# Performance work log

Measured on AMD Instinct MI355X. Metric: run time of the kernel, lower is better.

The kernel has to match this reference:

```python
import jax, jax.numpy as jnp
import numpy as np

N, C, H, W = 8, 192, 64, 64
CQK = 24  # C // ratio with ratio=8


def setup_inputs() -> dict:
    key = jax.random.key(0)
    k1, k2, k3, k4 = jax.random.split(key, 4)
    x = jax.random.normal(k1, (N, C, H, W), dtype=jnp.float32)
    Wq = jax.random.normal(k2, (CQK, C), dtype=jnp.float32) * (1.0 / np.sqrt(C))
    Wk = jax.random.normal(k3, (CQK, C), dtype=jnp.float32) * (1.0 / np.sqrt(C))
    Wv = jax.random.normal(k4, (C, C), dtype=jnp.float32) * (1.0 / np.sqrt(C))
    return {"x": x, "Wq": Wq, "Wk": Wk, "Wv": Wv}


def reference(x, Wq, Wk, Wv):
    n, c, h, w = x.shape
    xf = x.reshape(n, c, h * w)                       # [n, C, L]
    q = jnp.einsum('oc,ncl->nol', Wq, xf)             # [n, CQK, L] (1x1 conv)
    k = jnp.einsum('oc,ncl->nol', Wk, xf)             # [n, CQK, L]
    v = jnp.einsum('oc,ncl->nol', Wv, xf)             # [n, C, L]
    # mask[n, l, m] = softmax_m( q[:, :, l] . k[:, :, m] )  -- no scaling in original
    scores = jnp.einsum('nol,nom->nlm', q, k)         # [n, L, L]
    mask = jax.nn.softmax(scores, axis=-1)
    # feat = v @ mask^T : feat[n, c, l] = sum_m v[n, c, m] * mask[n, l, m]
    feat = jnp.einsum('ncm,nlm->ncl', v, mask)
    return feat.reshape(n, c, h, w)
```

## Files before the change

### kernel.cpp

```cpp
#include <hip/hip_runtime.h>
#include <hip/hip_bf16.h>

#define L 4096
#define NB 8
#define C 192
#define CQK 24
#define DP 32
#define QBLK 64
#define KBLK 64
#define NT (L / KBLK)
#define BN 64
#define XS_W 200
#define LOG2E 1.4426950408889634f

typedef _Float16 half_t;
typedef __fp16 fp16x2 __attribute__((ext_vector_type(2)));
typedef __fp16 fp16x4 __attribute__((ext_vector_type(4)));
typedef _Float16 half8 __attribute__((ext_vector_type(8)));
typedef float f32x4 __attribute__((ext_vector_type(4)));


__global__ __launch_bounds__(256, 2) void proj_mfma(const float* __restrict__ x,
                                                    const float* __restrict__ Wq,
                                                    const float* __restrict__ Wk,
                                                    const float* __restrict__ Wv,
                                                    half_t* __restrict__ Qh,
                                                    half_t* __restrict__ Kh,
                                                    half_t* __restrict__ Vh) {
  __shared__ half_t Xs[BN][XS_W];
  __shared__ half_t Qt[BN][DP];
  __shared__ half_t Kt[BN][DP];

  int tid = threadIdx.x;
  int lane = tid & 63;
  int wave = tid >> 6;
  int li = lane & 15;
  int g = lane >> 4;

  int blk = blockIdx.x;
  int n = blk >> 6;
  int l0 = (blk & 63) * BN;

  const float* xbase = x + (size_t)n * C * L + l0;
#pragma unroll
  for (int it = 0; it < 12; ++it) {
    int fid = it * 256 + tid;
    int l4 = fid & 15;
    int c = fid >> 4;
    f32x4 v = *reinterpret_cast<const f32x4*>(xbase + (size_t)c * L + l4 * 4);
#pragma unroll
    for (int j = 0; j < 4; ++j) Xs[l4 * 4 + j][c] = (half_t)v[j];
  }
  __syncthreads();

  const float* rowp[4];
  bool rvalid[4];
#pragma unroll
  for (int mt = 0; mt < 4; ++mt) {
    int row = wave * 64 + mt * 16 + li;
    const float* p;
    bool v = true;
    if (row < 32) {
      v = row < CQK;
      p = Wq + (size_t)(v ? row : 0) * C;
    } else if (row < 64) {
      v = (row - 32) < CQK;
      p = Wk + (size_t)(v ? row - 32 : 0) * C;
    } else {
      p = Wv + (size_t)(row - 64) * C;
    }
    rowp[mt] = p;
    rvalid[mt] = v;
  }

  f32x4 acc[4][4];
#pragma unroll
  for (int mt = 0; mt < 4; ++mt)
#pragma unroll
    for (int nt = 0; nt < 4; ++nt) acc[mt][nt] = {0.f, 0.f, 0.f, 0.f};

  half8 az;
#pragma unroll
  for (int j = 0; j < 8; ++j) az[j] = (half_t)0.f;

#pragma unroll
  for (int kk = 0; kk < 6; ++kk) {
    half8 af[4];
#pragma unroll
    for (int mt = 0; mt < 4; ++mt) {
      const float* p = rowp[mt] + kk * 32 + g * 8;
      f32x4 w0 = *reinterpret_cast<const f32x4*>(p);
      f32x4 w1 = *reinterpret_cast<const f32x4*>(p + 4);
      half8 a;
#pragma unroll
      for (int j = 0; j < 4; ++j) {
        a[j] = (half_t)w0[j];
        a[4 + j] = (half_t)w1[j];
      }
      af[mt] = rvalid[mt] ? a : az;
    }
#pragma unroll
    for (int nt = 0; nt < 4; ++nt) {
      half8 b = *reinterpret_cast<const half8*>(&Xs[nt * 16 + li][kk * 32 + g * 8]);
#pragma unroll
      for (int mt = 0; mt < 4; ++mt)
        acc[mt][nt] = __builtin_amdgcn_mfma_f32_16x16x32_f16(af[mt], b, acc[mt][nt], 0, 0, 0);
    }
  }

  if (wave >= 1) {
#pragma unroll
    for (int mt = 0; mt < 4; ++mt)
#pragma unroll
      for (int nt = 0; nt < 4; ++nt)
#pragma unroll
        for (int r = 0; r < 4; ++r) {
          int c = (wave - 1) * 64 + mt * 16 + 4 * g + r;
          int l = nt * 16 + li;
          Vh[((size_t)n * C + c) * L + l0 + l] = (half_t)acc[mt][nt][r];
        }
  } else {
#pragma unroll
    for (int mt = 0; mt < 4; ++mt)
#pragma unroll
      for (int nt = 0; nt < 4; ++nt)
#pragma unroll
        for (int r = 0; r < 4; ++r) {
          int o = (mt & 1) * 16 + 4 * g + r;
          int l = nt * 16 + li;
          if (mt < 2) Qt[l][o] = (half_t)(acc[mt][nt][r] * LOG2E);
          else        Kt[l][o] = (half_t)acc[mt][nt][r];
        }
  }
  __syncthreads();

  if (tid < 128) {
    int which = tid >> 6;
    int l = tid & 63;
    const half8* src = reinterpret_cast<const half8*>(which ? &Kt[l][0] : &Qt[l][0]);
    half_t* dstp = (which ? Kh : Qh) + ((size_t)n * L + l0 + l) * DP;
    half8* dst = reinterpret_cast<half8*>(dstp);
#pragma unroll
    for (int i = 0; i < 4; ++i) dst[i] = src[i];
  }
}


struct SMemA {
  half_t P[2][QBLK][KBLK];
  float rs[2][QBLK];
  float Ls[QBLK];
};

__global__ __launch_bounds__(256, 2) void attn(const half_t* __restrict__ Qh,
                                               const half_t* __restrict__ Kh,
                                               const half_t* __restrict__ Vh,
                                               float* __restrict__ out) {
  __shared__ SMemA sm;

  const int tid = threadIdx.x;
  const int wave = tid >> 6;
  const int lane = tid & 63;
  const int li = lane & 15;
  const int g = lane >> 4;
  const int n = blockIdx.x;
  const int q0 = blockIdx.y * QBLK;
  const int c0 = wave * 48;
  const int swz = (li & 7) << 4;

  const half8 qfrag = *reinterpret_cast<const half8*>(
      Qh + ((size_t)(n * L + q0 + wave * 16 + li)) * DP + g * 8);

  const char* kptr = (const char*)(Kh + (size_t)n * L * DP) +
                     ((size_t)li * DP + g * 8) * 2;
  const char* vb[3];
  vb[0] = (const char*)(Vh + (size_t)n * C * L) +
          ((size_t)(c0 + li) * L + g * 8) * 2;
  vb[1] = vb[0] + (size_t)16 * L * 2;
  vb[2] = vb[0] + (size_t)32 * L * 2;

  f32x4 acc[3][4];
#pragma unroll
  for (int ct = 0; ct < 3; ++ct)
#pragma unroll
    for (int qt = 0; qt < 4; ++qt) acc[ct][qt] = {0.f, 0.f, 0.f, 0.f};

  float Lrow = 0.f;
  float coff = -28.f;

  half8 kA[4], vA[6], kB[4], vB[6];

  auto sm_write = [&](const f32x4(&s)[4], int par) {
    float p[4][4];
    float mx = -1.0e30f;
#pragma unroll
    for (int b = 0; b < 4; ++b) {
      mx = fmaxf(mx, fmaxf(fmaxf(s[b][0], s[b][1]), fmaxf(s[b][2], s[b][3])));
#pragma unroll
      for (int r = 0; r < 4; ++r) p[b][r] = __builtin_amdgcn_exp2f(s[b][r]);
    }
    float sc = 1.0f;
    if (__any((int)(mx > 15.f))) {
      float m2 = fmaxf(mx, __shfl_xor(mx, 16));
      m2 = fmaxf(m2, __shfl_xor(m2, 32));
      if (m2 > 15.f) {
        sc = __builtin_amdgcn_exp2f(-m2);
        Lrow *= sc;
        coff -= m2;
#pragma unroll
        for (int b = 0; b < 4; ++b)
#pragma unroll
          for (int r = 0; r < 4; ++r)
            p[b][r] = __builtin_amdgcn_exp2f(s[b][r] - m2);
      }
    }
#pragma unroll
    for (int b = 0; b < 4; ++b)
#pragma unroll
      for (int r = 0; r < 4; ++r) Lrow += p[b][r];

    char* prow = (char*)&sm.P[par][wave * 16 + li][0];
#pragma unroll
    for (int b = 0; b < 4; ++b) {
      fp16x2 lo = __builtin_amdgcn_cvt_pkrtz(p[b][0], p[b][1]);
      fp16x2 hi = __builtin_amdgcn_cvt_pkrtz(p[b][2], p[b][3]);
      fp16x4 h = __builtin_shufflevector(lo, hi, 0, 1, 2, 3);
      *reinterpret_cast<fp16x4*>(prow + ((b * 32 + 8 * g) ^ swz)) = h;
    }
    if (lane < 16) sm.rs[par][li * 4 + wave] = sc;
  };

  auto apply_rescale = [&](int par) {
    f32x4 f = *reinterpret_cast<const f32x4*>(&sm.rs[par][li * 4]);
    bool an = (f[0] != 1.f) | (f[1] != 1.f) | (f[2] != 1.f) | (f[3] != 1.f);
    if (__any((int)an)) {
#pragma unroll
      for (int ct = 0; ct < 3; ++ct)
#pragma unroll
        for (int qt = 0; qt < 4; ++qt) acc[ct][qt] *= f[qt];
    }
  };

  auto pv = [&](const half8(&vp)[6], int par) {
#pragma unroll
    for (int ch = 0; ch < 2; ++ch)
#pragma unroll
      for (int qt = 0; qt < 4; ++qt) {
        const char* prow = (const char*)&sm.P[par][qt * 16 + li][0];
        half8 pfrag = *reinterpret_cast<const half8*>(
            prow + ((ch * 64 + 16 * g) ^ swz));
#pragma unroll
        for (int ct = 0; ct < 3; ++ct)
          acc[ct][qt] = __builtin_amdgcn_mfma_f32_16x16x32_f16(
              vp[ct * 2 + ch], pfrag, acc[ct][qt], 0, 0, 0);
      }
  };

#pragma unroll
  for (int b = 0; b < 4; ++b)
    kA[b] = *reinterpret_cast<const half8*>(kptr + b * 1024);
  kptr += KBLK * DP * 2;
#pragma unroll
  for (int b = 0; b < 4; ++b)
    kB[b] = *reinterpret_cast<const half8*>(kptr + b * 1024);
  kptr += KBLK * DP * 2;
#pragma unroll
  for (int ct = 0; ct < 3; ++ct) {
    vA[ct * 2 + 0] = *reinterpret_cast<const half8*>(vb[ct]);
    vA[ct * 2 + 1] = *reinterpret_cast<const half8*>(vb[ct] + 64);
    vb[ct] += KBLK * 2;
  }
  {
    f32x4 cvec = {coff, coff, coff, coff};
    f32x4 s[4];
#pragma unroll
    for (int b = 0; b < 4; ++b)
      s[b] = __builtin_amdgcn_mfma_f32_16x16x32_f16(kA[b], qfrag, cvec, 0, 0, 0);
    sm_write(s, 0);
  }
  asm volatile("s_waitcnt lgkmcnt(0)\n\ts_barrier" ::: "memory");

  auto phase = [&](const half8(&kq)[4], const half8(&vp)[6], half8(&kd)[4],
                   half8(&vd)[6], int par, bool doK) {
    if (doK) {
#pragma unroll
      for (int b = 0; b < 4; ++b)
        kd[b] = *reinterpret_cast<const half8*>(kptr + b * 1024);
      kptr += KBLK * DP * 2;
    }
#pragma unroll
    for (int ct = 0; ct < 3; ++ct) {
      vd[ct * 2 + 0] = *reinterpret_cast<const half8*>(vb[ct]);
      vd[ct * 2 + 1] = *reinterpret_cast<const half8*>(vb[ct] + 64);
      vb[ct] += KBLK * 2;
    }

    f32x4 cvec = {coff, coff, coff, coff};
    f32x4 s[4];
#pragma unroll
    for (int b = 0; b < 4; ++b)
      s[b] = __builtin_amdgcn_mfma_f32_16x16x32_f16(kq[b], qfrag, cvec, 0, 0, 0);

    apply_rescale(par);
    sm_write(s, par ^ 1);
    pv(vp, par);

    asm volatile("s_waitcnt lgkmcnt(0)\n\ts_barrier" ::: "memory");
  };

  for (int t = 0; t < NT - 2; t += 2) {
    phase(kB, vA, kA, vB, 0, true);
    phase(kA, vB, kB, vA, 1, true);
  }
  phase(kB, vA, kA, vB, 0, false);

  apply_rescale(1);
  pv(vB, 1);

  float sum = Lrow;
  sum += __shfl_xor(sum, 16);
  sum += __shfl_xor(sum, 32);
  if (lane < 16) sm.Ls[li * 4 + wave] = sum;
  __syncthreads();

  f32x4 Lv = *reinterpret_cast<const f32x4*>(&sm.Ls[li * 4]);
  float inv[4];
#pragma unroll
  for (int qt = 0; qt < 4; ++qt) inv[qt] = 1.0f / Lv[qt];

#pragma unroll
  for (int ct = 0; ct < 3; ++ct)
#pragma unroll
    for (int qt = 0; qt < 4; ++qt)
#pragma unroll
      for (int r = 0; r < 4; ++r)
        out[((size_t)n * C + c0 + ct * 16 + 4 * g + r) * L + q0 + qt * 16 + li] =
            acc[ct][qt][r] * inv[qt];
}


extern "C" void kernel_launch(void* const* d_in, const int* in_sizes, int n_in,
                              void* d_out, int out_size, void* d_ws, size_t ws_size,
                              hipStream_t stream) {
  (void)in_sizes; (void)n_in; (void)out_size; (void)ws_size;
  const float* x = (const float*)d_in[0];
  const float* Wq = (const float*)d_in[1];
  const float* Wk = (const float*)d_in[2];
  const float* Wv = (const float*)d_in[3];
  float* out = (float*)d_out;

  half_t* Qh = (half_t*)d_ws;
  half_t* Kh = Qh + (size_t)NB * L * DP;
  half_t* Vh = Kh + (size_t)NB * L * DP;

  hipLaunchKernelGGL(proj_mfma, dim3(NB * (L / BN)), dim3(256), 0, stream,
                     x, Wq, Wk, Wv, Qh, Kh, Vh);
  hipLaunchKernelGGL(attn, dim3(NB, L / QBLK), dim3(256), 0, stream,
                     Qh, Kh, Vh, out);
}
```

Baseline: 142.6 us.

## Software-pipeline QK score MFMA one tile ahead of softmax and PV

Restructures the flash-attention main loop so the QK^T MFMA for the next key tile is issued a phase earlier, with scores kept in double-buffered sA/sB registers. The softmax for tile t then works on scores computed in the previous phase, which hides MFMA latency behind the exp and PV work. When a rescale happens, the already-computed next-tile scores are shifted by the new max offset to stay consistent. This costs more VGPRs for the extra score buffer and makes the prologue and epilogue more complex.

```diff
diff --git a/kernel.cpp b/kernel.cpp
--- a/kernel.cpp
+++ b/kernel.cpp
@@ -188,9 +188,31 @@
   float Lrow = 0.f;
   float coff = -28.f;
 
-  half8 kA[4], vA[6], kB[4], vB[6];
-
-  auto sm_write = [&](const f32x4(&s)[4], int par) {
+  half8 kA[4], kB[4], vA[6], vB[6];
+  f32x4 sA[4], sB[4];
+
+  auto loadKinto = [&](half8(&kd)[4]) {
+#pragma unroll
+    for (int b = 0; b < 4; ++b)
+      kd[b] = *reinterpret_cast<const half8*>(kptr + b * 1024);
+    kptr += KBLK * DP * 2;
+  };
+  auto loadVinto = [&](half8(&vd)[6]) {
+#pragma unroll
+    for (int ct = 0; ct < 3; ++ct) {
+      vd[ct * 2 + 0] = *reinterpret_cast<const half8*>(vb[ct]);
+      vd[ct * 2 + 1] = *reinterpret_cast<const half8*>(vb[ct] + 64);
+      vb[ct] += KBLK * 2;
+    }
+  };
+  auto qk = [&](const half8(&kq)[4], f32x4(&s)[4]) {
+    f32x4 cvec = {coff, coff, coff, coff};
+#pragma unroll
+    for (int b = 0; b < 4; ++b)
+      s[b] = __builtin_amdgcn_mfma_f32_16x16x32_f16(kq[b], qfrag, cvec, 0, 0, 0);
+  };
+
+  auto sm_write = [&](const f32x4(&s)[4], f32x4(&sn)[4], int par) {
     float p[4][4];
     float mx = -1.0e30f;
 #pragma unroll
@@ -210,8 +232,10 @@
 #pragma unroll
         for (int b = 0; b < 4; ++b)
 #pragma unroll
-          for (int r = 0; r < 4; ++r)
+          for (int r = 0; r < 4; ++r) {
             p[b][r] = __builtin_amdgcn_exp2f(s[b][r] - m2);
+            sn[b][r] -= m2;
+          }
       }
     }
 #pragma unroll
@@ -256,63 +280,35 @@
       }
   };
 
-#pragma unroll
-  for (int b = 0; b < 4; ++b)
-    kA[b] = *reinterpret_cast<const half8*>(kptr + b * 1024);
-  kptr += KBLK * DP * 2;
-#pragma unroll
-  for (int b = 0; b < 4; ++b)
-    kB[b] = *reinterpret_cast<const half8*>(kptr + b * 1024);
-  kptr += KBLK * DP * 2;
-#pragma unroll
-  for (int ct = 0; ct < 3; ++ct) {
-    vA[ct * 2 + 0] = *reinterpret_cast<const half8*>(vb[ct]);
-    vA[ct * 2 + 1] = *reinterpret_cast<const half8*>(vb[ct] + 64);
-    vb[ct] += KBLK * 2;
-  }
-  {
-    f32x4 cvec = {coff, coff, coff, coff};
-    f32x4 s[4];
-#pragma unroll
-    for (int b = 0; b < 4; ++b)
-      s[b] = __builtin_amdgcn_mfma_f32_16x16x32_f16(kA[b], qfrag, cvec, 0, 0, 0);
-    sm_write(s, 0);
-  }
+  loadKinto(kA);
+  loadKinto(kB);
+  qk(kA, sA);
+
+  loadKinto(kA);
+  loadVinto(vA);
+  qk(kB, sB);
+  sm_write(sA, sB, 0);
   asm volatile("s_waitcnt lgkmcnt(0)\n\ts_barrier" ::: "memory");
 
-  auto phase = [&](const half8(&kq)[4], const half8(&vp)[6], half8(&kd)[4],
-                   half8(&vd)[6], int par, bool doK) {
-    if (doK) {
-#pragma unroll
-      for (int b = 0; b < 4; ++b)
-        kd[b] = *reinterpret_cast<const half8*>(kptr + b * 1024);
-      kptr += KBLK * DP * 2;
-    }
-#pragma unroll
-    for (int ct = 0; ct < 3; ++ct) {
-      vd[ct * 2 + 0] = *reinterpret_cast<const half8*>(vb[ct]);
-      vd[ct * 2 + 1] = *reinterpret_cast<const half8*>(vb[ct] + 64);
-      vb[ct] += KBLK * 2;
-    }
-
-    f32x4 cvec = {coff, coff, coff, coff};
-    f32x4 s[4];
-#pragma unroll
-    for (int b = 0; b < 4; ++b)
-      s[b] = __builtin_amdgcn_mfma_f32_16x16x32_f16(kq[b], qfrag, cvec, 0, 0, 0);
-
-    apply_rescale(par);
-    sm_write(s, par ^ 1);
-    pv(vp, par);
-
+  auto phase = [&](const half8(&kq)[4], half8(&kd)[4], const half8(&vp)[6],
+                   half8(&vd)[6], const f32x4(&s_c)[4], f32x4(&s_n)[4],
+                   int parW, bool doK, bool doQK) {
+    if (doK) loadKinto(kd);
+    loadVinto(vd);
+    if (doQK) qk(kq, s_n);
+    apply_rescale(parW ^ 1);
+    sm_write(s_c, s_n, parW);
+    pv(vp, parW ^ 1);
     asm volatile("s_waitcnt lgkmcnt(0)\n\ts_barrier" ::: "memory");
   };
 
-  for (int t = 0; t < NT - 2; t += 2) {
-    phase(kB, vA, kA, vB, 0, true);
-    phase(kA, vB, kB, vA, 1, true);
-  }
-  phase(kB, vA, kA, vB, 0, false);
+  for (int t = 1; t <= NT - 5; t += 2) {
+    phase(kA, kB, vA, vB, sB, sA, 1, true, true);
+    phase(kB, kA, vB, vA, sA, sB, 0, true, true);
+  }
+  phase(kA, kB, vA, vB, sB, sA, 1, true, true);
+  phase(kB, kA, vB, vA, sA, sB, 0, false, true);
+  phase(kA, kB, vA, vB, sB, sA, 1, false, false);
 
   apply_rescale(1);
   pv(vB, 1);
```

Result: no change. 143.0 us (+0.3%).
